# Kernel optimization log

Hardware: AMD Instinct MI355X
Metric: run time of the kernel (lower is better)

The kernel has to match this reference:

```python
import jax, jax.numpy as jnp
import numpy as np

INPUT_SIZE = 256
HIDDEN_SIZE = 256

def setup_inputs() -> dict:
    key = jax.random.key(0)
    ks = jax.random.split(key, 10)
    B = 65536
    scale_in = 1.0 / np.sqrt(INPUT_SIZE)
    scale_h = 1.0 / np.sqrt(HIDDEN_SIZE)
    inp = {
        "x": jax.random.normal(ks[0], (B, INPUT_SIZE), dtype=jnp.float32),
        "h_prev": jax.random.normal(ks[1], (B, HIDDEN_SIZE), dtype=jnp.float32),
        # nn.Linear weights are [out, in]; torch computes x @ W.T
        "W_z": jax.random.uniform(ks[2], (HIDDEN_SIZE, INPUT_SIZE), jnp.float32, -scale_in, scale_in),
        "U_z": jax.random.uniform(ks[3], (HIDDEN_SIZE, HIDDEN_SIZE), jnp.float32, -scale_h, scale_h),
        "b_z": jnp.zeros((HIDDEN_SIZE,), dtype=jnp.float32),
        "W_a": jax.random.uniform(ks[4], (HIDDEN_SIZE, INPUT_SIZE), jnp.float32, -scale_in, scale_in),
        "U_a": jax.random.uniform(ks[5], (HIDDEN_SIZE, HIDDEN_SIZE), jnp.float32, -scale_h, scale_h),
        "v_a": jax.random.normal(ks[6], (HIDDEN_SIZE,), dtype=jnp.float32),
        "W_h": jax.random.uniform(ks[7], (HIDDEN_SIZE, INPUT_SIZE), jnp.float32, -scale_in, scale_in),
        "U_h": jax.random.uniform(ks[8], (HIDDEN_SIZE, HIDDEN_SIZE), jnp.float32, -scale_h, scale_h),
        "b_h": jnp.zeros((HIDDEN_SIZE,), dtype=jnp.float32),
    }
    return inp

def reference(x, h_prev, W_z, U_z, b_z, W_a, U_a, v_a, W_h, U_h, b_h):
    # update gate
    z_t = jax.nn.sigmoid(x @ W_z.T + h_prev @ U_z.T + b_z)  # [B, H]
    # attention-based reset replacement
    attention_input = jnp.tanh(x @ W_a.T + h_prev @ U_a.T)   # [B, H]
    attention_weights = jax.nn.softmax(attention_input * v_a, axis=-1)
    attended_h = attention_weights * h_prev                   # [B, H]
    # candidate state
    h_tilde = jnp.tanh(x @ W_h.T + attended_h @ U_h.T + b_h)  # [B, H]
    # blend
    h_t = (1.0 - z_t) * h_prev + z_t * h_tilde
    return h_t
```

## Files before the change

### kernel.cpp

```cpp
#include <hip/hip_runtime.h>

typedef __attribute__((ext_vector_type(8))) short  short8v;
typedef __attribute__((ext_vector_type(4))) float  float4v;

#define BDIM 512

__device__ ushort g_w[3 * 8 * 16 * 2 * 64 * 8];

__device__ __forceinline__ ushort f2bf(float f) {
  unsigned u = __float_as_uint(f);
  u += 0x7fffu + ((u >> 16) & 1u);
  return (ushort)(u >> 16);
}
__device__ __forceinline__ float bf2f(ushort s) {
  return __uint_as_float(((unsigned)s) << 16);
}

__global__ __launch_bounds__(256) void conv_w(
    const float* __restrict__ Wz, const float* __restrict__ Uz,
    const float* __restrict__ Wa, const float* __restrict__ Ua,
    const float* __restrict__ Wh, const float* __restrict__ Uh)
{
  int tid = blockIdx.x * 256 + threadIdx.x;
  int p   = tid >> 14;
  int kb  = (tid >> 11) & 7;
  int c16 = (tid >> 7) & 15;
  int s   = (tid >> 6) & 1;
  int l   = tid & 63;
  const float* W = (p == 0) ? Wz : (p == 1) ? Wa : Wh;
  const float* U = (p == 0) ? Uz : (p == 1) ? Ua : Uh;
  int col = c16 * 16 + (l & 15);
  int k0  = kb * 64 + s * 32 + ((l >> 4) << 3);
  const float* src = (k0 < 256) ? (W + col * 256 + k0) : (U + col * 256 + (k0 - 256));
  uint pk[4];
#pragma unroll
  for (int jj = 0; jj < 4; ++jj) {
    float v0 = src[jj * 2], v1 = src[jj * 2 + 1];
    pk[jj] = (uint)f2bf(v0) | ((uint)f2bf(v1) << 16);
  }
  *reinterpret_cast<uint4*>(&g_w[(size_t)tid * 8]) = make_uint4(pk[0], pk[1], pk[2], pk[3]);
}

__global__ __launch_bounds__(BDIM)
void gru_fused(
    const float* __restrict__ x,  const float* __restrict__ hp,
    const float* __restrict__ bz, const float* __restrict__ va,
    const float* __restrict__ bh, float* __restrict__ out)
{
  __shared__ __align__(16) ushort sA[64 * 512];
  __shared__ __align__(16) float  sRed[2][64 * 8];

  const int tid  = threadIdx.x;
  const int w    = tid >> 6;
  const int lane = tid & 63;
  const int g4   = lane >> 4;
  const int l15  = lane & 15;
  const int sxor = l15 & 7;
  const int rowBlk = blockIdx.x << 6;

  const ushort* wbase = g_w + (size_t)(w * 2048) + (size_t)lane * 8;
  short8v bB[2][2];
  auto loadBs = [&](int t, short8v* b) {
    const ushort* pb = wbase + ((size_t)(t >> 1) << 14) + (size_t)((t & 1) << 9);
    b[0] = *reinterpret_cast<const short8v*>(pb);
    b[1] = *reinterpret_cast<const short8v*>(pb + 1024);
  };

  loadBs(0, bB[0]);

  {
    const float4* xq = reinterpret_cast<const float4*>(x)  + (size_t)rowBlk * 64;
    const float4* hq = reinterpret_cast<const float4*>(hp) + (size_t)rowBlk * 64;
#pragma unroll
    for (int i = 0; i < 16; ++i) {
      int q   = tid + i * BDIM;
      int row = q >> 7;
      int qc  = q & 127;
      float4 v = (qc < 64) ? xq[row * 64 + qc] : hq[row * 64 + qc - 64];
      int kE  = qc << 2;
      int swz = (kE >> 3) ^ (row & 7);
      ushort4 pk4;
      pk4.x = f2bf(v.x); pk4.y = f2bf(v.y); pk4.z = f2bf(v.z); pk4.w = f2bf(v.w);
      *reinterpret_cast<ushort4*>((char*)sA + (row << 10) + (swz << 4) + ((kE & 7) << 1)) = pk4;
    }
  }
  __syncthreads();

  float4v acc[4][2];
  uint    zp[4][2][2];
  uint    hvp[4][2][2];

  for (int p = 0; p < 3; ++p) {
#pragma unroll
    for (int m = 0; m < 4; ++m)
#pragma unroll
      for (int r = 0; r < 2; ++r)
        acc[m][r] = (float4v){0.f, 0.f, 0.f, 0.f};

#pragma unroll
    for (int kb = 0; kb < 8; ++kb) {
#pragma unroll
      for (int s = 0; s < 2; ++s) {
        if ((kb * 2 + s < 15) || (p < 2))
          loadBs(p * 16 + kb * 2 + s + 1, bB[s ^ 1]);
        short8v afr[4];
#pragma unroll
        for (int m = 0; m < 4; ++m) {
          int row = m * 16 + l15;
          int swz = (kb * 8 + s * 4 + g4) ^ sxor;
          afr[m] = *reinterpret_cast<const short8v*>((const char*)sA + (row << 10) + (swz << 4));
        }
#pragma unroll
        for (int m = 0; m < 4; ++m)
#pragma unroll
          for (int r = 0; r < 2; ++r)
            acc[m][r] = __builtin_amdgcn_mfma_f32_16x16x32_bf16(afr[m], bB[s][r], acc[m][r], 0, 0, 0);
      }
    }

    if (p == 0) {
#pragma unroll
      for (int r = 0; r < 2; ++r) {
        float b = bz[(w << 5) + (r << 4) + l15];
#pragma unroll
        for (int m = 0; m < 4; ++m)
#pragma unroll
          for (int jj = 0; jj < 2; ++jj) {
            float z0 = 1.f / (1.f + __expf(-(acc[m][r][2 * jj]     + b)));
            float z1 = 1.f / (1.f + __expf(-(acc[m][r][2 * jj + 1] + b)));
            zp[m][r][jj] = (uint)f2bf(z0) | ((uint)f2bf(z1) << 16);
          }
      }
    } else if (p == 1) {
      float vav[2];
      vav[0] = va[(w << 5) + l15];
      vav[1] = va[(w << 5) + 16 + l15];
#pragma unroll
      for (int m = 0; m < 4; ++m)
#pragma unroll
        for (int r = 0; r < 2; ++r)
#pragma unroll
          for (int j = 0; j < 4; ++j) {
            float s = acc[m][r][j];
            float t = 1.f - 2.f / (__expf(2.f * s) + 1.f);
            acc[m][r][j] = t * vav[r];
          }
      float mx[4][4];
#pragma unroll
      for (int m = 0; m < 4; ++m)
#pragma unroll
        for (int j = 0; j < 4; ++j) {
          float v = fmaxf(acc[m][0][j], acc[m][1][j]);
          v = fmaxf(v, __shfl_xor(v, 1));
          v = fmaxf(v, __shfl_xor(v, 2));
          v = fmaxf(v, __shfl_xor(v, 4));
          v = fmaxf(v, __shfl_xor(v, 8));
          mx[m][j] = v;
        }
      if (l15 == 0) {
#pragma unroll
        for (int m = 0; m < 4; ++m)
#pragma unroll
          for (int j = 0; j < 4; ++j)
            sRed[0][((m * 16 + g4 * 4 + j) << 3) + w] = mx[m][j];
      }
      __syncthreads();
      float rmax[4][4];
#pragma unroll
      for (int m = 0; m < 4; ++m)
#pragma unroll
        for (int j = 0; j < 4; ++j) {
          int row = m * 16 + g4 * 4 + j;
          const float4* pr = reinterpret_cast<const float4*>(&sRed[0][row << 3]);
          float4 a = pr[0], b = pr[1];
          rmax[m][j] = fmaxf(fmaxf(fmaxf(a.x, a.y), fmaxf(a.z, a.w)),
                             fmaxf(fmaxf(b.x, b.y), fmaxf(b.z, b.w)));
        }
#pragma unroll
      for (int m = 0; m < 4; ++m)
#pragma unroll
        for (int j = 0; j < 4; ++j) {
          float e0 = __expf(acc[m][0][j] - rmax[m][j]);
          float e1 = __expf(acc[m][1][j] - rmax[m][j]);
          acc[m][0][j] = e0; acc[m][1][j] = e1;
          float sm = e0 + e1;
          sm += __shfl_xor(sm, 1);
          sm += __shfl_xor(sm, 2);
          sm += __shfl_xor(sm, 4);
          sm += __shfl_xor(sm, 8);
          if (l15 == 0) sRed[1][((m * 16 + g4 * 4 + j) << 3) + w] = sm;
        }
#pragma unroll
      for (int m = 0; m < 4; ++m)
#pragma unroll
        for (int r = 0; r < 2; ++r)
#pragma unroll
          for (int jj = 0; jj < 2; ++jj) {
            int row0 = m * 16 + g4 * 4 + 2 * jj;
            int row1 = row0 + 1;
            int cs0  = (32 + (w << 2) + (r << 1) + (l15 >> 3)) ^ (row0 & 7);
            int cs1  = (32 + (w << 2) + (r << 1) + (l15 >> 3)) ^ (row1 & 7);
            uint h0 = sA[(row0 << 9) + (cs0 << 3) + sxor];
            uint h1 = sA[(row1 << 9) + (cs1 << 3) + sxor];
            hvp[m][r][jj] = h0 | (h1 << 16);
          }
      __syncthreads();
#pragma unroll
      for (int m = 0; m < 4; ++m)
#pragma unroll
        for (int j = 0; j < 4; ++j) {
          int row = m * 16 + g4 * 4 + j;
          const float4* pr = reinterpret_cast<const float4*>(&sRed[1][row << 3]);
          float4 a = pr[0], b = pr[1];
          float s = (a.x + a.y) + (a.z + a.w) + (b.x + b.y) + (b.z + b.w);
          float inv = 1.f / s;
#pragma unroll
          for (int r = 0; r < 2; ++r) {
            uint hw = hvp[m][r][j >> 1];
            float hval = bf2f((ushort)((j & 1) ? (hw >> 16) : (hw & 0xffffu)));
            float at = acc[m][r][j] * inv * hval;
            int cs = (32 + (w << 2) + (r << 1) + (l15 >> 3)) ^ (row & 7);
            sA[(row << 9) + (cs << 3) + sxor] = f2bf(at);
          }
        }
      __syncthreads();
    } else {
#pragma unroll
      for (int r = 0; r < 2; ++r) {
        float b = bh[(w << 5) + (r << 4) + l15];
#pragma unroll
        for (int m = 0; m < 4; ++m)
#pragma unroll
          for (int j = 0; j < 4; ++j) {
            float s  = acc[m][r][j] + b;
            float ht = 1.f - 2.f / (__expf(2.f * s) + 1.f);
            uint zw  = zp[m][r][j >> 1];
            float z  = bf2f((ushort)((j & 1) ? (zw >> 16) : (zw & 0xffffu)));
            uint hw  = hvp[m][r][j >> 1];
            float h0 = bf2f((ushort)((j & 1) ? (hw >> 16) : (hw & 0xffffu)));
            float res = (1.f - z) * h0 + z * ht;
            int row = m * 16 + g4 * 4 + j;
            out[(size_t)(rowBlk + row) * 256 + (w << 5) + (r << 4) + l15] = res;
          }
      }
    }
  }
}

extern "C" void kernel_launch(void* const* d_in, const int* in_sizes, int n_in,
                              void* d_out, int out_size, void* d_ws, size_t ws_size,
                              hipStream_t stream)
{
  const float* x  = (const float*)d_in[0];
  const float* hp = (const float*)d_in[1];
  const float* Wz = (const float*)d_in[2];
  const float* Uz = (const float*)d_in[3];
  const float* bz = (const float*)d_in[4];
  const float* Wa = (const float*)d_in[5];
  const float* Ua = (const float*)d_in[6];
  const float* va = (const float*)d_in[7];
  const float* Wh = (const float*)d_in[8];
  const float* Uh = (const float*)d_in[9];
  const float* bh = (const float*)d_in[10];
  float* out = (float*)d_out;

  conv_w<<<dim3(192), dim3(256), 0, stream>>>(Wz, Uz, Wa, Ua, Wh, Uh);
  gru_fused<<<dim3(1024), dim3(BDIM), 0, stream>>>(x, hp, bz, va, bh, out);
}
```

Baseline: 373.4 us.

## Fuse update-gate and attention GEMMs into one pass sharing A fragments

The z and attention projections now run in a single K loop. Each A fragment read from shared memory feeds MFMAs for both weight sets, which halves the LDS A reads for those two GEMMs and interleaves two independent MFMA chains. The candidate GEMM runs afterwards, with its first weight tile prefetched at the end of the fused loop. Launch bounds now request 4 blocks per multiprocessor. Keeping two accumulator sets and two B buffers live raises register pressure, and this could conflict with the occupancy hint and cause spills.

```diff
diff --git a/kernel.cpp b/kernel.cpp
--- a/kernel.cpp
+++ b/kernel.cpp
@@ -41,7 +41,7 @@
   *reinterpret_cast<uint4*>(&g_w[(size_t)tid * 8]) = make_uint4(pk[0], pk[1], pk[2], pk[3]);
 }
 
-__global__ __launch_bounds__(BDIM)
+__global__ __launch_bounds__(BDIM, 4)
 void gru_fused(
     const float* __restrict__ x,  const float* __restrict__ hp,
     const float* __restrict__ bz, const float* __restrict__ va,
@@ -59,14 +59,16 @@
   const int rowBlk = blockIdx.x << 6;
 
   const ushort* wbase = g_w + (size_t)(w * 2048) + (size_t)lane * 8;
-  short8v bB[2][2];
-  auto loadBs = [&](int t, short8v* b) {
-    const ushort* pb = wbase + ((size_t)(t >> 1) << 14) + (size_t)((t & 1) << 9);
+  short8v bZ[2][2], bA[2][2], bH[2][2];
+  auto loadS = [&](int p, int t, short8v* b) {
+    const ushort* pb = wbase + (size_t)p * 131072
+                     + ((size_t)(t >> 1) << 14) + ((size_t)(t & 1) << 9);
     b[0] = *reinterpret_cast<const short8v*>(pb);
     b[1] = *reinterpret_cast<const short8v*>(pb + 1024);
   };
 
-  loadBs(0, bB[0]);
+  loadS(0, 0, bZ[0]);
+  loadS(1, 0, bA[0]);
 
   {
     const float4* xq = reinterpret_cast<const float4*>(x)  + (size_t)rowBlk * 64;
@@ -86,164 +88,191 @@
   }
   __syncthreads();
 
-  float4v acc[4][2];
-  uint    zp[4][2][2];
-  uint    hvp[4][2][2];
-
-  for (int p = 0; p < 3; ++p) {
+  float4v accZ[4][2], accA[4][2];
+#pragma unroll
+  for (int m = 0; m < 4; ++m)
+#pragma unroll
+    for (int r = 0; r < 2; ++r) {
+      accZ[m][r] = (float4v){0.f, 0.f, 0.f, 0.f};
+      accA[m][r] = (float4v){0.f, 0.f, 0.f, 0.f};
+    }
+
+#pragma unroll
+  for (int kb = 0; kb < 8; ++kb)
+#pragma unroll
+    for (int s = 0; s < 2; ++s) {
+      const int t = kb * 2 + s;
+      if (t < 15) { loadS(0, t + 1, bZ[s ^ 1]); loadS(1, t + 1, bA[s ^ 1]); }
+      else        { loadS(2, 0, bH[0]); }
+      short8v afr[4];
+#pragma unroll
+      for (int m = 0; m < 4; ++m) {
+        int row = m * 16 + l15;
+        int swz = (kb * 8 + s * 4 + g4) ^ sxor;
+        afr[m] = *reinterpret_cast<const short8v*>((const char*)sA + (row << 10) + (swz << 4));
+      }
+#pragma unroll
+      for (int m = 0; m < 4; ++m)
+#pragma unroll
+        for (int r = 0; r < 2; ++r) {
+          accZ[m][r] = __builtin_amdgcn_mfma_f32_16x16x32_bf16(afr[m], bZ[s][r], accZ[m][r], 0, 0, 0);
+          accA[m][r] = __builtin_amdgcn_mfma_f32_16x16x32_bf16(afr[m], bA[s][r], accA[m][r], 0, 0, 0);
+        }
+    }
+
+  uint zp[4][2][2];
+#pragma unroll
+  for (int r = 0; r < 2; ++r) {
+    float b = bz[(w << 5) + (r << 4) + l15];
+#pragma unroll
+    for (int m = 0; m < 4; ++m)
+#pragma unroll
+      for (int jj = 0; jj < 2; ++jj) {
+        float z0 = 1.f / (1.f + __expf(-(accZ[m][r][2 * jj]     + b)));
+        float z1 = 1.f / (1.f + __expf(-(accZ[m][r][2 * jj + 1] + b)));
+        zp[m][r][jj] = (uint)f2bf(z0) | ((uint)f2bf(z1) << 16);
+      }
+  }
+
+  uint hvp[4][2][2];
+  {
+    float vav[2];
+    vav[0] = va[(w << 5) + l15];
+    vav[1] = va[(w << 5) + 16 + l15];
 #pragma unroll
     for (int m = 0; m < 4; ++m)
 #pragma unroll
       for (int r = 0; r < 2; ++r)
-        acc[m][r] = (float4v){0.f, 0.f, 0.f, 0.f};
-
-#pragma unroll
-    for (int kb = 0; kb < 8; ++kb) {
-#pragma unroll
-      for (int s = 0; s < 2; ++s) {
-        if ((kb * 2 + s < 15) || (p < 2))
-          loadBs(p * 16 + kb * 2 + s + 1, bB[s ^ 1]);
-        short8v afr[4];
-#pragma unroll
-        for (int m = 0; m < 4; ++m) {
-          int row = m * 16 + l15;
-          int swz = (kb * 8 + s * 4 + g4) ^ sxor;
-          afr[m] = *reinterpret_cast<const short8v*>((const char*)sA + (row << 10) + (swz << 4));
-        }
-#pragma unroll
-        for (int m = 0; m < 4; ++m)
-#pragma unroll
-          for (int r = 0; r < 2; ++r)
-            acc[m][r] = __builtin_amdgcn_mfma_f32_16x16x32_bf16(afr[m], bB[s][r], acc[m][r], 0, 0, 0);
-      }
-    }
-
-    if (p == 0) {
-#pragma unroll
-      for (int r = 0; r < 2; ++r) {
-        float b = bz[(w << 5) + (r << 4) + l15];
-#pragma unroll
-        for (int m = 0; m < 4; ++m)
-#pragma unroll
-          for (int jj = 0; jj < 2; ++jj) {
-            float z0 = 1.f / (1.f + __expf(-(acc[m][r][2 * jj]     + b)));
-            float z1 = 1.f / (1.f + __expf(-(acc[m][r][2 * jj + 1] + b)));
-            zp[m][r][jj] = (uint)f2bf(z0) | ((uint)f2bf(z1) << 16);
-          }
-      }
-    } else if (p == 1) {
-      float vav[2];
-      vav[0] = va[(w << 5) + l15];
-      vav[1] = va[(w << 5) + 16 + l15];
+#pragma unroll
+        for (int j = 0; j < 4; ++j) {
+          float s = accA[m][r][j];
+          float t = 1.f - 2.f / (__expf(2.f * s) + 1.f);
+          accA[m][r][j] = t * vav[r];
+        }
+    float mx[4][4];
+#pragma unroll
+    for (int m = 0; m < 4; ++m)
+#pragma unroll
+      for (int j = 0; j < 4; ++j) {
+        float v = fmaxf(accA[m][0][j], accA[m][1][j]);
+        v = fmaxf(v, __shfl_xor(v, 1));
+        v = fmaxf(v, __shfl_xor(v, 2));
+        v = fmaxf(v, __shfl_xor(v, 4));
+        v = fmaxf(v, __shfl_xor(v, 8));
+        mx[m][j] = v;
+      }
+    if (l15 == 0) {
 #pragma unroll
       for (int m = 0; m < 4; ++m)
 #pragma unroll
+        for (int j = 0; j < 4; ++j)
+          sRed[0][((m * 16 + g4 * 4 + j) << 3) + w] = mx[m][j];
+    }
+    __syncthreads();
+    float rmax[4][4];
+#pragma unroll
+    for (int m = 0; m < 4; ++m)
+#pragma unroll
+      for (int j = 0; j < 4; ++j) {
+        int row = m * 16 + g4 * 4 + j;
+        const float4* pr = reinterpret_cast<const float4*>(&sRed[0][row << 3]);
+        float4 a = pr[0], b = pr[1];
+        rmax[m][j] = fmaxf(fmaxf(fmaxf(a.x, a.y), fmaxf(a.z, a.w)),
+                           fmaxf(fmaxf(b.x, b.y), fmaxf(b.z, b.w)));
+      }
+#pragma unroll
+    for (int m = 0; m < 4; ++m)
+#pragma unroll
+      for (int j = 0; j < 4; ++j) {
+        float e0 = __expf(accA[m][0][j] - rmax[m][j]);
+        float e1 = __expf(accA[m][1][j] - rmax[m][j]);
+        accA[m][0][j] = e0; accA[m][1][j] = e1;
+        float sm = e0 + e1;
+        sm += __shfl_xor(sm, 1);
+        sm += __shfl_xor(sm, 2);
+        sm += __shfl_xor(sm, 4);
+        sm += __shfl_xor(sm, 8);
+        if (l15 == 0) sRed[1][((m * 16 + g4 * 4 + j) << 3) + w] = sm;
+      }
+#pragma unroll
+    for (int m = 0; m < 4; ++m)
+#pragma unroll
+      for (int r = 0; r < 2; ++r)
+#pragma unroll
+        for (int jj = 0; jj < 2; ++jj) {
+          int row0 = m * 16 + g4 * 4 + 2 * jj;
+          int row1 = row0 + 1;
+          int cs0  = (32 + (w << 2) + (r << 1) + (l15 >> 3)) ^ (row0 & 7);
+          int cs1  = (32 + (w << 2) + (r << 1) + (l15 >> 3)) ^ (row1 & 7);
+          uint h0 = sA[(row0 << 9) + (cs0 << 3) + sxor];
+          uint h1 = sA[(row1 << 9) + (cs1 << 3) + sxor];
+          hvp[m][r][jj] = h0 | (h1 << 16);
+        }
+    __syncthreads();
+#pragma unroll
+    for (int m = 0; m < 4; ++m)
+#pragma unroll
+      for (int j = 0; j < 4; ++j) {
+        int row = m * 16 + g4 * 4 + j;
+        const float4* pr = reinterpret_cast<const float4*>(&sRed[1][row << 3]);
+        float4 a = pr[0], b = pr[1];
+        float s = (a.x + a.y) + (a.z + a.w) + (b.x + b.y) + (b.z + b.w);
+        float inv = 1.f / s;
+#pragma unroll
+        for (int r = 0; r < 2; ++r) {
+          uint hw = hvp[m][r][j >> 1];
+          float hval = bf2f((ushort)((j & 1) ? (hw >> 16) : (hw & 0xffffu)));
+          float at = accA[m][r][j] * inv * hval;
+          int cs = (32 + (w << 2) + (r << 1) + (l15 >> 3)) ^ (row & 7);
+          sA[(row << 9) + (cs << 3) + sxor] = f2bf(at);
+        }
+      }
+    __syncthreads();
+  }
+
+  float4v accH[4][2];
+#pragma unroll
+  for (int m = 0; m < 4; ++m)
+#pragma unroll
+    for (int r = 0; r < 2; ++r)
+      accH[m][r] = (float4v){0.f, 0.f, 0.f, 0.f};
+#pragma unroll
+  for (int kb = 0; kb < 8; ++kb)
+#pragma unroll
+    for (int s = 0; s < 2; ++s) {
+      const int t = kb * 2 + s;
+      if (t < 15) loadS(2, t + 1, bH[s ^ 1]);
+      short8v afr[4];
+#pragma unroll
+      for (int m = 0; m < 4; ++m) {
+        int row = m * 16 + l15;
+        int swz = (kb * 8 + s * 4 + g4) ^ sxor;
+        afr[m] = *reinterpret_cast<const short8v*>((const char*)sA + (row << 10) + (swz << 4));
+      }
+#pragma unroll
+      for (int m = 0; m < 4; ++m)
+#pragma unroll
         for (int r = 0; r < 2; ++r)
-#pragma unroll
-          for (int j = 0; j < 4; ++j) {
-            float s = acc[m][r][j];
-            float t = 1.f - 2.f / (__expf(2.f * s) + 1.f);
-            acc[m][r][j] = t * vav[r];
-          }
-      float mx[4][4];
-#pragma unroll
-      for (int m = 0; m < 4; ++m)
-#pragma unroll
-        for (int j = 0; j < 4; ++j) {
-          float v = fmaxf(acc[m][0][j], acc[m][1][j]);
-          v = fmaxf(v, __shfl_xor(v, 1));
-          v = fmaxf(v, __shfl_xor(v, 2));
-          v = fmaxf(v, __shfl_xor(v, 4));
-          v = fmaxf(v, __shfl_xor(v, 8));
-          mx[m][j] = v;
-        }
-      if (l15 == 0) {
-#pragma unroll
-        for (int m = 0; m < 4; ++m)
-#pragma unroll
-          for (int j = 0; j < 4; ++j)
-            sRed[0][((m * 16 + g4 * 4 + j) << 3) + w] = mx[m][j];
-      }
-      __syncthreads();
-      float rmax[4][4];
-#pragma unroll
-      for (int m = 0; m < 4; ++m)
-#pragma unroll
-        for (int j = 0; j < 4; ++j) {
-          int row = m * 16 + g4 * 4 + j;
-          const float4* pr = reinterpret_cast<const float4*>(&sRed[0][row << 3]);
-          float4 a = pr[0], b = pr[1];
-          rmax[m][j] = fmaxf(fmaxf(fmaxf(a.x, a.y), fmaxf(a.z, a.w)),
-                             fmaxf(fmaxf(b.x, b.y), fmaxf(b.z, b.w)));
-        }
-#pragma unroll
-      for (int m = 0; m < 4; ++m)
-#pragma unroll
-        for (int j = 0; j < 4; ++j) {
-          float e0 = __expf(acc[m][0][j] - rmax[m][j]);
-          float e1 = __expf(acc[m][1][j] - rmax[m][j]);
-          acc[m][0][j] = e0; acc[m][1][j] = e1;
-          float sm = e0 + e1;
-          sm += __shfl_xor(sm, 1);
-          sm += __shfl_xor(sm, 2);
-          sm += __shfl_xor(sm, 4);
-          sm += __shfl_xor(sm, 8);
-          if (l15 == 0) sRed[1][((m * 16 + g4 * 4 + j) << 3) + w] = sm;
-        }
-#pragma unroll
-      for (int m = 0; m < 4; ++m)
-#pragma unroll
-        for (int r = 0; r < 2; ++r)
-#pragma unroll
-          for (int jj = 0; jj < 2; ++jj) {
-            int row0 = m * 16 + g4 * 4 + 2 * jj;
-            int row1 = row0 + 1;
-            int cs0  = (32 + (w << 2) + (r << 1) + (l15 >> 3)) ^ (row0 & 7);
-            int cs1  = (32 + (w << 2) + (r << 1) + (l15 >> 3)) ^ (row1 & 7);
-            uint h0 = sA[(row0 << 9) + (cs0 << 3) + sxor];
-            uint h1 = sA[(row1 << 9) + (cs1 << 3) + sxor];
-            hvp[m][r][jj] = h0 | (h1 << 16);
-          }
-      __syncthreads();
-#pragma unroll
-      for (int m = 0; m < 4; ++m)
-#pragma unroll
-        for (int j = 0; j < 4; ++j) {
-          int row = m * 16 + g4 * 4 + j;
-          const float4* pr = reinterpret_cast<const float4*>(&sRed[1][row << 3]);
-          float4 a = pr[0], b = pr[1];
-          float s = (a.x + a.y) + (a.z + a.w) + (b.x + b.y) + (b.z + b.w);
-          float inv = 1.f / s;
-#pragma unroll
-          for (int r = 0; r < 2; ++r) {
-            uint hw = hvp[m][r][j >> 1];
-            float hval = bf2f((ushort)((j & 1) ? (hw >> 16) : (hw & 0xffffu)));
-            float at = acc[m][r][j] * inv * hval;
-            int cs = (32 + (w << 2) + (r << 1) + (l15 >> 3)) ^ (row & 7);
-            sA[(row << 9) + (cs << 3) + sxor] = f2bf(at);
-          }
-        }
-      __syncthreads();
-    } else {
-#pragma unroll
-      for (int r = 0; r < 2; ++r) {
-        float b = bh[(w << 5) + (r << 4) + l15];
-#pragma unroll
-        for (int m = 0; m < 4; ++m)
-#pragma unroll
-          for (int j = 0; j < 4; ++j) {
-            float s  = acc[m][r][j] + b;
-            float ht = 1.f - 2.f / (__expf(2.f * s) + 1.f);
-            uint zw  = zp[m][r][j >> 1];
-            float z  = bf2f((ushort)((j & 1) ? (zw >> 16) : (zw & 0xffffu)));
-            uint hw  = hvp[m][r][j >> 1];
-            float h0 = bf2f((ushort)((j & 1) ? (hw >> 16) : (hw & 0xffffu)));
-            float res = (1.f - z) * h0 + z * ht;
-            int row = m * 16 + g4 * 4 + j;
-            out[(size_t)(rowBlk + row) * 256 + (w << 5) + (r << 4) + l15] = res;
-          }
-      }
-    }
+          accH[m][r] = __builtin_amdgcn_mfma_f32_16x16x32_bf16(afr[m], bH[s][r], accH[m][r], 0, 0, 0);
+    }
+
+#pragma unroll
+  for (int r = 0; r < 2; ++r) {
+    float b = bh[(w << 5) + (r << 4) + l15];
+#pragma unroll
+    for (int m = 0; m < 4; ++m)
+#pragma unroll
+      for (int j = 0; j < 4; ++j) {
+        float s  = accH[m][r][j] + b;
+        float ht = 1.f - 2.f / (__expf(2.f * s) + 1.f);
+        uint zw  = zp[m][r][j >> 1];
+        float z  = bf2f((ushort)((j & 1) ? (zw >> 16) : (zw & 0xffffu)));
+        uint hw  = hvp[m][r][j >> 1];
+        float h0 = bf2f((ushort)((j & 1) ? (hw >> 16) : (hw & 0xffffu)));
+        float res = (1.f - z) * h0 + z * ht;
+        int row = m * 16 + g4 * 4 + j;
+        out[(size_t)(rowBlk + row) * 256 + (w << 5) + (r << 4) + l15] = res;
+      }
   }
 }
 
```

Result: faster. 348.0 us (-6.8%).

## Use 16 waves per block and fuse z/a GEMMs into one K loop

Applied to the files above, without the earlier changes.

The block grows from 8 to 16 waves, so each wave owns 16 output columns instead of 32. The z-gate and attention GEMMs are interleaved in a single K loop that shares the A-fragment LDS reads, and the candidate GEMM runs in its own loop. The softmax reduction buffers widen to 16 waves. This is meant to raise latency hiding and MFMA issue density per CU, at the cost of larger cross-wave softmax reductions and more register-pressure constraints from launch_bounds(1024, 4).

```diff
diff --git a/kernel.cpp b/kernel.cpp
--- a/kernel.cpp
+++ b/kernel.cpp
@@ -3,7 +3,7 @@
 typedef __attribute__((ext_vector_type(8))) short  short8v;
 typedef __attribute__((ext_vector_type(4))) float  float4v;
 
-#define BDIM 512
+#define BDIM 1024
 
 __device__ ushort g_w[3 * 8 * 16 * 2 * 64 * 8];
 
@@ -41,38 +41,41 @@
   *reinterpret_cast<uint4*>(&g_w[(size_t)tid * 8]) = make_uint4(pk[0], pk[1], pk[2], pk[3]);
 }
 
-__global__ __launch_bounds__(BDIM)
+__global__ __launch_bounds__(BDIM, 4)
 void gru_fused(
     const float* __restrict__ x,  const float* __restrict__ hp,
     const float* __restrict__ bz, const float* __restrict__ va,
     const float* __restrict__ bh, float* __restrict__ out)
 {
   __shared__ __align__(16) ushort sA[64 * 512];
-  __shared__ __align__(16) float  sRed[2][64 * 8];
+  __shared__ __align__(16) float  sRed[2][64 * 16];
 
   const int tid  = threadIdx.x;
-  const int w    = tid >> 6;
+  const int wv   = tid >> 6;
   const int lane = tid & 63;
   const int g4   = lane >> 4;
   const int l15  = lane & 15;
   const int sxor = l15 & 7;
+  const int col  = (wv << 4) + l15;
   const int rowBlk = blockIdx.x << 6;
 
-  const ushort* wbase = g_w + (size_t)(w * 2048) + (size_t)lane * 8;
-  short8v bB[2][2];
-  auto loadBs = [&](int t, short8v* b) {
-    const ushort* pb = wbase + ((size_t)(t >> 1) << 14) + (size_t)((t & 1) << 9);
-    b[0] = *reinterpret_cast<const short8v*>(pb);
-    b[1] = *reinterpret_cast<const short8v*>(pb + 1024);
+  const ushort* wbase = g_w + (size_t)(wv << 10) + (size_t)(lane << 3);
+  const ushort* pZ = wbase;
+  const ushort* pA = wbase + 131072;
+  const ushort* pH = wbase + 262144;
+  auto ld = [&](const ushort* px, int t) -> short8v {
+    return *reinterpret_cast<const short8v*>(px + ((size_t)(t >> 1) << 13) * 2 + ((size_t)(t & 1) << 9));
   };
 
-  loadBs(0, bB[0]);
+  short8v bZ0 = ld(pZ, 0), bA0 = ld(pA, 0);
+  short8v bZ1 = ld(pZ, 1), bA1 = ld(pA, 1);
+  short8v bH0, bH1;
 
   {
     const float4* xq = reinterpret_cast<const float4*>(x)  + (size_t)rowBlk * 64;
     const float4* hq = reinterpret_cast<const float4*>(hp) + (size_t)rowBlk * 64;
 #pragma unroll
-    for (int i = 0; i < 16; ++i) {
+    for (int i = 0; i < 8; ++i) {
       int q   = tid + i * BDIM;
       int row = q >> 7;
       int qc  = q & 127;
@@ -86,164 +89,192 @@
   }
   __syncthreads();
 
-  float4v acc[4][2];
-  uint    zp[4][2][2];
-  uint    hvp[4][2][2];
-
-  for (int p = 0; p < 3; ++p) {
-#pragma unroll
-    for (int m = 0; m < 4; ++m)
-#pragma unroll
-      for (int r = 0; r < 2; ++r)
-        acc[m][r] = (float4v){0.f, 0.f, 0.f, 0.f};
-
-#pragma unroll
-    for (int kb = 0; kb < 8; ++kb) {
-#pragma unroll
-      for (int s = 0; s < 2; ++s) {
-        if ((kb * 2 + s < 15) || (p < 2))
-          loadBs(p * 16 + kb * 2 + s + 1, bB[s ^ 1]);
-        short8v afr[4];
-#pragma unroll
-        for (int m = 0; m < 4; ++m) {
-          int row = m * 16 + l15;
-          int swz = (kb * 8 + s * 4 + g4) ^ sxor;
-          afr[m] = *reinterpret_cast<const short8v*>((const char*)sA + (row << 10) + (swz << 4));
-        }
-#pragma unroll
-        for (int m = 0; m < 4; ++m)
-#pragma unroll
-          for (int r = 0; r < 2; ++r)
-            acc[m][r] = __builtin_amdgcn_mfma_f32_16x16x32_bf16(afr[m], bB[s][r], acc[m][r], 0, 0, 0);
-      }
-    }
-
-    if (p == 0) {
-#pragma unroll
-      for (int r = 0; r < 2; ++r) {
-        float b = bz[(w << 5) + (r << 4) + l15];
-#pragma unroll
-        for (int m = 0; m < 4; ++m)
-#pragma unroll
-          for (int jj = 0; jj < 2; ++jj) {
-            float z0 = 1.f / (1.f + __expf(-(acc[m][r][2 * jj]     + b)));
-            float z1 = 1.f / (1.f + __expf(-(acc[m][r][2 * jj + 1] + b)));
-            zp[m][r][jj] = (uint)f2bf(z0) | ((uint)f2bf(z1) << 16);
-          }
-      }
-    } else if (p == 1) {
-      float vav[2];
-      vav[0] = va[(w << 5) + l15];
-      vav[1] = va[(w << 5) + 16 + l15];
+  float4v accZ[4], accA[4];
+#pragma unroll
+  for (int m = 0; m < 4; ++m) {
+    accZ[m] = (float4v){0.f, 0.f, 0.f, 0.f};
+    accA[m] = (float4v){0.f, 0.f, 0.f, 0.f};
+  }
+
+  for (int kb = 0; kb < 8; ++kb) {
+    short8v afr[4];
+#pragma unroll
+    for (int m = 0; m < 4; ++m) {
+      int swz = (kb * 8 + g4) ^ sxor;
+      afr[m] = *reinterpret_cast<const short8v*>(
+          (const char*)sA + ((m * 16 + l15) << 10) + (swz << 4));
+    }
+#pragma unroll
+    for (int m = 0; m < 4; ++m) {
+      accZ[m] = __builtin_amdgcn_mfma_f32_16x16x32_bf16(afr[m], bZ0, accZ[m], 0, 0, 0);
+      accA[m] = __builtin_amdgcn_mfma_f32_16x16x32_bf16(afr[m], bA0, accA[m], 0, 0, 0);
+    }
+    if (kb < 7) { bZ0 = ld(pZ, 2 * kb + 2); bA0 = ld(pA, 2 * kb + 2); }
+    else        { bH0 = ld(pH, 0); }
+#pragma unroll
+    for (int m = 0; m < 4; ++m) {
+      int swz = (kb * 8 + 4 + g4) ^ sxor;
+      afr[m] = *reinterpret_cast<const short8v*>(
+          (const char*)sA + ((m * 16 + l15) << 10) + (swz << 4));
+    }
+#pragma unroll
+    for (int m = 0; m < 4; ++m) {
+      accZ[m] = __builtin_amdgcn_mfma_f32_16x16x32_bf16(afr[m], bZ1, accZ[m], 0, 0, 0);
+      accA[m] = __builtin_amdgcn_mfma_f32_16x16x32_bf16(afr[m], bA1, accA[m], 0, 0, 0);
+    }
+    if (kb < 7) { bZ1 = ld(pZ, 2 * kb + 3); bA1 = ld(pA, 2 * kb + 3); }
+    else        { bH1 = ld(pH, 1); }
+  }
+
+  uint zp[4][2];
+  {
+    float b = bz[col];
+#pragma unroll
+    for (int m = 0; m < 4; ++m)
+#pragma unroll
+      for (int jj = 0; jj < 2; ++jj) {
+        float z0 = 1.f / (1.f + __expf(-(accZ[m][2 * jj]     + b)));
+        float z1 = 1.f / (1.f + __expf(-(accZ[m][2 * jj + 1] + b)));
+        zp[m][jj] = (uint)f2bf(z0) | ((uint)f2bf(z1) << 16);
+      }
+  }
+
+  uint hvp[4][2];
+  {
+    float vav = va[col];
+#pragma unroll
+    for (int m = 0; m < 4; ++m)
+#pragma unroll
+      for (int j = 0; j < 4; ++j) {
+        float s = accA[m][j];
+        float t = 1.f - 2.f / (__expf(2.f * s) + 1.f);
+        accA[m][j] = t * vav;
+      }
+    float mx[4][4];
+#pragma unroll
+    for (int m = 0; m < 4; ++m)
+#pragma unroll
+      for (int j = 0; j < 4; ++j) {
+        float v = accA[m][j];
+        v = fmaxf(v, __shfl_xor(v, 1));
+        v = fmaxf(v, __shfl_xor(v, 2));
+        v = fmaxf(v, __shfl_xor(v, 4));
+        v = fmaxf(v, __shfl_xor(v, 8));
+        mx[m][j] = v;
+      }
+    if (l15 == 0) {
 #pragma unroll
       for (int m = 0; m < 4; ++m)
 #pragma unroll
-        for (int r = 0; r < 2; ++r)
-#pragma unroll
-          for (int j = 0; j < 4; ++j) {
-            float s = acc[m][r][j];
-            float t = 1.f - 2.f / (__expf(2.f * s) + 1.f);
-            acc[m][r][j] = t * vav[r];
-          }
-      float mx[4][4];
-#pragma unroll
-      for (int m = 0; m < 4; ++m)
-#pragma unroll
-        for (int j = 0; j < 4; ++j) {
-          float v = fmaxf(acc[m][0][j], acc[m][1][j]);
-          v = fmaxf(v, __shfl_xor(v, 1));
-          v = fmaxf(v, __shfl_xor(v, 2));
-          v = fmaxf(v, __shfl_xor(v, 4));
-          v = fmaxf(v, __shfl_xor(v, 8));
-          mx[m][j] = v;
-        }
-      if (l15 == 0) {
-#pragma unroll
-        for (int m = 0; m < 4; ++m)
-#pragma unroll
-          for (int j = 0; j < 4; ++j)
-            sRed[0][((m * 16 + g4 * 4 + j) << 3) + w] = mx[m][j];
-      }
-      __syncthreads();
-      float rmax[4][4];
-#pragma unroll
-      for (int m = 0; m < 4; ++m)
-#pragma unroll
-        for (int j = 0; j < 4; ++j) {
-          int row = m * 16 + g4 * 4 + j;
-          const float4* pr = reinterpret_cast<const float4*>(&sRed[0][row << 3]);
-          float4 a = pr[0], b = pr[1];
-          rmax[m][j] = fmaxf(fmaxf(fmaxf(a.x, a.y), fmaxf(a.z, a.w)),
-                             fmaxf(fmaxf(b.x, b.y), fmaxf(b.z, b.w)));
-        }
-#pragma unroll
-      for (int m = 0; m < 4; ++m)
-#pragma unroll
-        for (int j = 0; j < 4; ++j) {
-          float e0 = __expf(acc[m][0][j] - rmax[m][j]);
-          float e1 = __expf(acc[m][1][j] - rmax[m][j]);
-          acc[m][0][j] = e0; acc[m][1][j] = e1;
-          float sm = e0 + e1;
-          sm += __shfl_xor(sm, 1);
-          sm += __shfl_xor(sm, 2);
-          sm += __shfl_xor(sm, 4);
-          sm += __shfl_xor(sm, 8);
-          if (l15 == 0) sRed[1][((m * 16 + g4 * 4 + j) << 3) + w] = sm;
-        }
-#pragma unroll
-      for (int m = 0; m < 4; ++m)
-#pragma unroll
-        for (int r = 0; r < 2; ++r)
-#pragma unroll
-          for (int jj = 0; jj < 2; ++jj) {
-            int row0 = m * 16 + g4 * 4 + 2 * jj;
-            int row1 = row0 + 1;
-            int cs0  = (32 + (w << 2) + (r << 1) + (l15 >> 3)) ^ (row0 & 7);
-            int cs1  = (32 + (w << 2) + (r << 1) + (l15 >> 3)) ^ (row1 & 7);
-            uint h0 = sA[(row0 << 9) + (cs0 << 3) + sxor];
-            uint h1 = sA[(row1 << 9) + (cs1 << 3) + sxor];
-            hvp[m][r][jj] = h0 | (h1 << 16);
-          }
-      __syncthreads();
-#pragma unroll
-      for (int m = 0; m < 4; ++m)
-#pragma unroll
-        for (int j = 0; j < 4; ++j) {
-          int row = m * 16 + g4 * 4 + j;
-          const float4* pr = reinterpret_cast<const float4*>(&sRed[1][row << 3]);
-          float4 a = pr[0], b = pr[1];
-          float s = (a.x + a.y) + (a.z + a.w) + (b.x + b.y) + (b.z + b.w);
-          float inv = 1.f / s;
-#pragma unroll
-          for (int r = 0; r < 2; ++r) {
-            uint hw = hvp[m][r][j >> 1];
-            float hval = bf2f((ushort)((j & 1) ? (hw >> 16) : (hw & 0xffffu)));
-            float at = acc[m][r][j] * inv * hval;
-            int cs = (32 + (w << 2) + (r << 1) + (l15 >> 3)) ^ (row & 7);
-            sA[(row << 9) + (cs << 3) + sxor] = f2bf(at);
-          }
-        }
-      __syncthreads();
-    } else {
-#pragma unroll
-      for (int r = 0; r < 2; ++r) {
-        float b = bh[(w << 5) + (r << 4) + l15];
-#pragma unroll
-        for (int m = 0; m < 4; ++m)
-#pragma unroll
-          for (int j = 0; j < 4; ++j) {
-            float s  = acc[m][r][j] + b;
-            float ht = 1.f - 2.f / (__expf(2.f * s) + 1.f);
-            uint zw  = zp[m][r][j >> 1];
-            float z  = bf2f((ushort)((j & 1) ? (zw >> 16) : (zw & 0xffffu)));
-            uint hw  = hvp[m][r][j >> 1];
-            float h0 = bf2f((ushort)((j & 1) ? (hw >> 16) : (hw & 0xffffu)));
-            float res = (1.f - z) * h0 + z * ht;
-            int row = m * 16 + g4 * 4 + j;
-            out[(size_t)(rowBlk + row) * 256 + (w << 5) + (r << 4) + l15] = res;
-          }
-      }
-    }
+        for (int j = 0; j < 4; ++j)
+          sRed[0][((m * 16 + g4 * 4 + j) << 4) + wv] = mx[m][j];
+    }
+    __syncthreads();
+    float rmax[4][4];
+#pragma unroll
+    for (int m = 0; m < 4; ++m)
+#pragma unroll
+      for (int j = 0; j < 4; ++j) {
+        int row = m * 16 + g4 * 4 + j;
+        const float4* pr = reinterpret_cast<const float4*>(&sRed[0][row << 4]);
+        float4 a = pr[0], b = pr[1], c = pr[2], d = pr[3];
+        float v01 = fmaxf(fmaxf(a.x, a.y), fmaxf(a.z, a.w));
+        float v23 = fmaxf(fmaxf(b.x, b.y), fmaxf(b.z, b.w));
+        float v45 = fmaxf(fmaxf(c.x, c.y), fmaxf(c.z, c.w));
+        float v67 = fmaxf(fmaxf(d.x, d.y), fmaxf(d.z, d.w));
+        rmax[m][j] = fmaxf(fmaxf(v01, v23), fmaxf(v45, v67));
+      }
+#pragma unroll
+    for (int m = 0; m < 4; ++m)
+#pragma unroll
+      for (int j = 0; j < 4; ++j) {
+        float e = __expf(accA[m][j] - rmax[m][j]);
+        accA[m][j] = e;
+        float sm = e;
+        sm += __shfl_xor(sm, 1);
+        sm += __shfl_xor(sm, 2);
+        sm += __shfl_xor(sm, 4);
+        sm += __shfl_xor(sm, 8);
+        if (l15 == 0) sRed[1][((m * 16 + g4 * 4 + j) << 4) + wv] = sm;
+      }
+#pragma unroll
+    for (int m = 0; m < 4; ++m)
+#pragma unroll
+      for (int jj = 0; jj < 2; ++jj) {
+        int row0 = m * 16 + g4 * 4 + 2 * jj;
+        int row1 = row0 + 1;
+        int ch   = 32 + (wv << 1) + (l15 >> 3);
+        int cs0  = ch ^ (row0 & 7);
+        int cs1  = ch ^ (row1 & 7);
+        uint h0 = sA[(row0 << 9) + (cs0 << 3) + sxor];
+        uint h1 = sA[(row1 << 9) + (cs1 << 3) + sxor];
+        hvp[m][jj] = h0 | (h1 << 16);
+      }
+    __syncthreads();
+#pragma unroll
+    for (int m = 0; m < 4; ++m)
+#pragma unroll
+      for (int j = 0; j < 4; ++j) {
+        int row = m * 16 + g4 * 4 + j;
+        const float4* pr = reinterpret_cast<const float4*>(&sRed[1][row << 4]);
+        float4 a = pr[0], b = pr[1], c = pr[2], d = pr[3];
+        float s = ((a.x + a.y) + (a.z + a.w)) + ((b.x + b.y) + (b.z + b.w))
+                + ((c.x + c.y) + (c.z + c.w)) + ((d.x + d.y) + (d.z + d.w));
+        float inv = 1.f / s;
+        uint hw = hvp[m][j >> 1];
+        float hval = bf2f((ushort)((j & 1) ? (hw >> 16) : (hw & 0xffffu)));
+        float at = accA[m][j] * inv * hval;
+        int ch = 32 + (wv << 1) + (l15 >> 3);
+        int cs = ch ^ (row & 7);
+        sA[(row << 9) + (cs << 3) + sxor] = f2bf(at);
+      }
+    __syncthreads();
+  }
+
+  float4v accH[4];
+#pragma unroll
+  for (int m = 0; m < 4; ++m)
+    accH[m] = (float4v){0.f, 0.f, 0.f, 0.f};
+  for (int kb = 0; kb < 8; ++kb) {
+    short8v afr[4];
+#pragma unroll
+    for (int m = 0; m < 4; ++m) {
+      int swz = (kb * 8 + g4) ^ sxor;
+      afr[m] = *reinterpret_cast<const short8v*>(
+          (const char*)sA + ((m * 16 + l15) << 10) + (swz << 4));
+    }
+#pragma unroll
+    for (int m = 0; m < 4; ++m)
+      accH[m] = __builtin_amdgcn_mfma_f32_16x16x32_bf16(afr[m], bH0, accH[m], 0, 0, 0);
+    if (kb < 7) bH0 = ld(pH, 2 * kb + 2);
+#pragma unroll
+    for (int m = 0; m < 4; ++m) {
+      int swz = (kb * 8 + 4 + g4) ^ sxor;
+      afr[m] = *reinterpret_cast<const short8v*>(
+          (const char*)sA + ((m * 16 + l15) << 10) + (swz << 4));
+    }
+#pragma unroll
+    for (int m = 0; m < 4; ++m)
+      accH[m] = __builtin_amdgcn_mfma_f32_16x16x32_bf16(afr[m], bH1, accH[m], 0, 0, 0);
+    if (kb < 7) bH1 = ld(pH, 2 * kb + 3);
+  }
+
+  {
+    float b = bh[col];
+#pragma unroll
+    for (int m = 0; m < 4; ++m)
+#pragma unroll
+      for (int j = 0; j < 4; ++j) {
+        float s  = accH[m][j] + b;
+        float ht = 1.f - 2.f / (__expf(2.f * s) + 1.f);
+        uint zw  = zp[m][j >> 1];
+        float z  = bf2f((ushort)((j & 1) ? (zw >> 16) : (zw & 0xffffu)));
+        uint hw  = hvp[m][j >> 1];
+        float h0 = bf2f((ushort)((j & 1) ? (hw >> 16) : (hw & 0xffffu)));
+        float res = (1.f - z) * h0 + z * ht;
+        int row = m * 16 + g4 * 4 + j;
+        out[(size_t)(rowBlk + row) * 256 + col] = res;
+      }
   }
 }
 
```

Result: slower. 626.4 us (+67.8%).
